# Kernel tuning notes

Hardware: AMD Instinct MI355X
Metric: run time of the kernel (lower is better)

Reference implementation:

```python
import jax, jax.numpy as jnp
import numpy as np

HEADS = 16
D_MODEL = 1024
GROUP = 4
SEQ = 2048
HEAD_DIM = D_MODEL // HEADS          # 64
KV_HEADS = HEADS // GROUP            # 4


def rope_tables(head_dim, seq_len, base=10000.0):
    # NOTE: faithful to source: exp = -2*arange(0,d,2)/d  (steps of 2 -> base^{-4j/d})
    exp = -2.0 * jnp.arange(0, head_dim, 2, dtype=jnp.float32) / head_dim
    thetas = jnp.power(base, exp)                       # [d/2]
    m = jnp.arange(seq_len, dtype=jnp.float32)          # [S]
    freq = jnp.outer(m, thetas)                         # [S, d/2]
    return jnp.cos(freq), jnp.sin(freq)


def apply_rope(x, cos, sin):
    # x: [B,S,H,D]; complex rotation on consecutive pairs
    B, S, H, D = x.shape
    xr = x.reshape(B, S, H, D // 2, 2)
    x0, x1 = xr[..., 0], xr[..., 1]
    c = cos[None, :S, None, :]
    s = sin[None, :S, None, :]
    out = jnp.stack([x0 * c - x1 * s, x0 * s + x1 * c], axis=-1)
    return out.reshape(B, S, H, D)


def setup_inputs() -> dict:
    key = jax.random.key(0)
    ks = jax.random.split(key, 8)
    B = 1
    q = jax.random.normal(ks[0], (B, SEQ, D_MODEL), dtype=jnp.float32)
    k = jax.random.normal(ks[1], (B, SEQ, D_MODEL), dtype=jnp.float32)
    v = jax.random.normal(ks[2], (B, SEQ, D_MODEL), dtype=jnp.float32)
    mask = jnp.tril(jnp.ones((SEQ, SEQ), dtype=jnp.int32))[None]  # causal [B,S,S]
    sc = 0.02
    Wq = jax.random.normal(ks[3], (D_MODEL, D_MODEL), dtype=jnp.float32) * sc
    Wk = jax.random.normal(ks[4], (D_MODEL, D_MODEL // GROUP), dtype=jnp.float32) * sc
    Wv = jax.random.normal(ks[5], (D_MODEL, D_MODEL // GROUP), dtype=jnp.float32) * sc
    Wo = jax.random.normal(ks[6], (D_MODEL, D_MODEL), dtype=jnp.float32) * sc
    bq = jnp.zeros((D_MODEL,), jnp.float32)
    bk = jnp.zeros((D_MODEL // GROUP,), jnp.float32)
    bv = jnp.zeros((D_MODEL // GROUP,), jnp.float32)
    bo = jnp.zeros((D_MODEL,), jnp.float32)
    return {"q": q, "k": k, "v": v, "mask": mask, "Wq": Wq, "bq": bq,
            "Wk": Wk, "bk": bk, "Wv": Wv, "bv": bv, "Wo": Wo, "bo": bo}


def reference(q, k, v, mask, Wq, bq, Wk, bk, Wv, bv, Wo, bo):
    B, S, _ = q.shape
    cos, sin = rope_tables(HEAD_DIM, S)
    qh = (q @ Wq + bq).reshape(B, S, HEADS, HEAD_DIM)
    kh = (k @ Wk + bk).reshape(B, S, KV_HEADS, HEAD_DIM)
    vh = (v @ Wv + bv).reshape(B, S, KV_HEADS, HEAD_DIM)
    qh = apply_rope(qh, cos, sin)
    kh = apply_rope(kh, cos, sin)
    qh = qh.transpose(0, 2, 1, 3)                       # [B,H,S,D]
    kh = kh.transpose(0, 2, 1, 3)                       # [B,Hkv,S,D]
    vh = vh.transpose(0, 2, 1, 3)
    # torch .repeat tiles: query head j attends kv head j % KV_HEADS
    kh = jnp.tile(kh, (1, GROUP, 1, 1))                 # [B,H,S,D]
    vh = jnp.tile(vh, (1, GROUP, 1, 1))
    scores = jnp.einsum('bhqd,bhkd->bhqk', qh, kh) / jnp.sqrt(
        jnp.asarray(HEAD_DIM, dtype=qh.dtype))
    scores = jnp.where(mask[:, None, :, :] == 0, -jnp.inf, scores)
    attn = jax.nn.softmax(scores, axis=-1)
    out = jnp.einsum('bhqk,bhkd->bhqd', attn, vh)
    out = out.transpose(0, 2, 1, 3).reshape(B, S, D_MODEL)
    return out @ Wo + bo
```

## Files before the change

kernel.cpp:

```cpp
#include <hip/hip_runtime.h>
#include <hip/hip_bf16.h>
#include <math.h>


#define SEQ 2048
#define DM 1024
#define HD 64

using u16 = unsigned short;
typedef __attribute__((ext_vector_type(8))) short bf16x8;
typedef __attribute__((ext_vector_type(4))) float f32x4;

#define QSCALE 0.18033688011112042f

__device__ __forceinline__ u16 f2b(float f) {
    union { float f; unsigned int i; } v; v.f = f;
    unsigned int u = v.i;
    return (u16)((u + 0x7fffu + ((u >> 16) & 1u)) >> 16);
}
__device__ __forceinline__ u16 f2b_fast(float f) {
    union { float f; unsigned int i; } v; v.f = f;
    return (u16)((v.i + 0x8000u) >> 16);
}

__global__ __launch_bounds__(256) void prep_kernel(
    const float* __restrict__ qin, const float* __restrict__ kin, const float* __restrict__ vin,
    const float* __restrict__ Wq, const float* __restrict__ Wk,
    const float* __restrict__ Wv, const float* __restrict__ Wo,
    u16* __restrict__ Xq, u16* __restrict__ Xk, u16* __restrict__ Xv,
    u16* __restrict__ Wt, u16* __restrict__ wot)
{
    const int b = blockIdx.x;
    const int t = threadIdx.x;

    if (b < 640) {
        __shared__ short T[64][72];
        const float* W; u16* dst; int N, t0, rowoff;
        if (b < 256)      { W = Wq; dst = Wt;  N = 1024; t0 = b;       rowoff = 0; }
        else if (b < 320) { W = Wk; dst = Wt;  N = 256;  t0 = b - 256; rowoff = 1024; }
        else if (b < 384) { W = Wv; dst = Wt;  N = 256;  t0 = b - 320; rowoff = 1280; }
        else              { W = Wo; dst = wot; N = 1024; t0 = b - 384; rowoff = 0; }
        const int ntn = N >> 6;
        const int k0 = (t0 / ntn) * 64, n0 = (t0 % ntn) * 64;
        const int r = t >> 4, c4 = (t & 15) * 4;
        #pragma unroll
        for (int rr = 0; rr < 4; ++rr) {
            const int k = r + rr * 16;
            float4 w4 = *reinterpret_cast<const float4*>(W + (size_t)(k0 + k) * N + n0 + c4);
            T[c4 + 0][k] = (short)f2b(w4.x);
            T[c4 + 1][k] = (short)f2b(w4.y);
            T[c4 + 2][k] = (short)f2b(w4.z);
            T[c4 + 3][k] = (short)f2b(w4.w);
        }
        __syncthreads();
        const int n = t >> 2, ck = (t & 3) * 16;
        u16* dp = dst + (size_t)(rowoff + n0 + n) * DM + k0 + ck;
        *reinterpret_cast<bf16x8*>(dp)     = *reinterpret_cast<const bf16x8*>(&T[n][ck]);
        *reinterpret_cast<bf16x8*>(dp + 8) = *reinterpret_cast<const bf16x8*>(&T[n][ck + 8]);
    } else {
        const int idx = b - 640;
        const int which = idx >> 8;
        const int ib = idx & 255;
        const float* src = (which == 0) ? qin : (which == 1) ? kin : vin;
        u16* dst = (which == 0) ? Xq : (which == 1) ? Xk : Xv;
        const size_t base = (size_t)ib * 8192 + (size_t)t * 32;
        #pragma unroll
        for (int c = 0; c < 4; ++c) {
            float4 x0 = *reinterpret_cast<const float4*>(src + base + c * 8);
            float4 x1 = *reinterpret_cast<const float4*>(src + base + c * 8 + 4);
            bf16x8 o;
            o[0] = (short)f2b(x0.x); o[1] = (short)f2b(x0.y);
            o[2] = (short)f2b(x0.z); o[3] = (short)f2b(x0.w);
            o[4] = (short)f2b(x1.x); o[5] = (short)f2b(x1.y);
            o[6] = (short)f2b(x1.z); o[7] = (short)f2b(x1.w);
            *reinterpret_cast<bf16x8*>(dst + base + c * 8) = o;
        }
    }
}

__global__ __launch_bounds__(256) void proj_mfma(
    const u16* __restrict__ Xq, const u16* __restrict__ Xk, const u16* __restrict__ Xv,
    const u16* __restrict__ Wt,
    const float* __restrict__ bq, const float* __restrict__ bk, const float* __restrict__ bv,
    u16* __restrict__ Qr, u16* __restrict__ Kr, u16* __restrict__ Vrt)
{
    const int n0 = blockIdx.x * 64, m0 = blockIdx.y * 64;
    const int zone = (n0 < 1024) ? 0 : (n0 < 1280) ? 1 : 2;
    const u16* __restrict__ Az = (zone == 0) ? Xq : (zone == 1) ? Xk : Xv;

    __shared__ short As[2][64][72];
    __shared__ short Bs[2][64][72];

    const int t = threadIdx.x;
    const int w = t >> 6, lane = t & 63, lm = lane & 15, quad = lane >> 4;
    const int sr = t >> 2, sc = (t & 3) * 16;

    f32x4 acc[4] = { {0,0,0,0}, {0,0,0,0}, {0,0,0,0}, {0,0,0,0} };

    const u16* ap_ = Az + (size_t)(m0 + sr) * DM + sc;
    const u16* bp_ = Wt + (size_t)(n0 + sr) * DM + sc;
    bf16x8 aR0 = *reinterpret_cast<const bf16x8*>(ap_);
    bf16x8 aR1 = *reinterpret_cast<const bf16x8*>(ap_ + 8);
    bf16x8 bR0 = *reinterpret_cast<const bf16x8*>(bp_);
    bf16x8 bR1 = *reinterpret_cast<const bf16x8*>(bp_ + 8);

    for (int k0 = 0; k0 < DM; k0 += 64) {
        const int buf = (k0 >> 6) & 1;
        *reinterpret_cast<bf16x8*>(&As[buf][sr][sc])     = aR0;
        *reinterpret_cast<bf16x8*>(&As[buf][sr][sc + 8]) = aR1;
        *reinterpret_cast<bf16x8*>(&Bs[buf][sr][sc])     = bR0;
        *reinterpret_cast<bf16x8*>(&Bs[buf][sr][sc + 8]) = bR1;
        if (k0 + 64 < DM) {
            aR0 = *reinterpret_cast<const bf16x8*>(ap_ + k0 + 64);
            aR1 = *reinterpret_cast<const bf16x8*>(ap_ + k0 + 72);
            bR0 = *reinterpret_cast<const bf16x8*>(bp_ + k0 + 64);
            bR1 = *reinterpret_cast<const bf16x8*>(bp_ + k0 + 72);
        }
        __syncthreads();
        bf16x8 af0 = *reinterpret_cast<const bf16x8*>(&As[buf][16 * w + lm][quad * 8]);
        bf16x8 af1 = *reinterpret_cast<const bf16x8*>(&As[buf][16 * w + lm][32 + quad * 8]);
        #pragma unroll
        for (int nb = 0; nb < 4; ++nb) {
            bf16x8 b0 = *reinterpret_cast<const bf16x8*>(&Bs[buf][16 * nb + lm][quad * 8]);
            bf16x8 b1 = *reinterpret_cast<const bf16x8*>(&Bs[buf][16 * nb + lm][32 + quad * 8]);
            acc[nb] = __builtin_amdgcn_mfma_f32_16x16x32_bf16(af0, b0, acc[nb], 0, 0, 0);
            acc[nb] = __builtin_amdgcn_mfma_f32_16x16x32_bf16(af1, b1, acc[nb], 0, 0, 0);
        }
        __syncthreads();
    }

    const float* __restrict__ bias = (zone == 0) ? bq : (zone == 1) ? bk : bv;
    const int nbase = (zone == 0) ? n0 : (zone == 1) ? (n0 - 1024) : (n0 - 1280);
    const int head = nbase >> 6;
    #pragma unroll
    for (int nb = 0; nb < 4; ++nb) {
        const int d = 16 * nb + lm;
        const float bvv = bias[nbase + d];
        float vals[4];
        #pragma unroll
        for (int r = 0; r < 4; ++r) vals[r] = acc[nb][r] + bvv;
        if (zone != 2) {
            const int pi = d >> 1;
            const float theta = exp2f(-0.8304820237f * (float)pi);
            const bool odd = (lm & 1);
            const float sca = (zone == 0) ? QSCALE : 1.0f;
            u16* op = (zone == 0 ? Qr : Kr) + (size_t)head * SEQ * HD;
            #pragma unroll
            for (int r = 0; r < 4; ++r) {
                const int m = m0 + 16 * w + quad * 4 + r;
                float sn, cs;
                sincosf((float)m * theta, &sn, &cs);
                float x  = vals[r];
                float xp = __shfl_xor(x, 1);
                float o  = (odd ? (xp * sn + x * cs) : (x * cs - xp * sn)) * sca;
                op[(size_t)m * HD + d] = f2b(o);
            }
        } else {
            u16* vp = Vrt + ((size_t)head * HD + d) * SEQ;
            #pragma unroll
            for (int r = 0; r < 4; ++r) {
                const int m = m0 + 16 * w + quad * 4 + r;
                const int within = m & 63;
                const int pos = (m & ~63) + 4 * (within & 15) + (within >> 4);
                vp[pos] = f2b(vals[r]);
            }
        }
    }
}

__global__ __launch_bounds__(512) void attn_mfma(
    const u16* __restrict__ Qr, const u16* __restrict__ Kr, const u16* __restrict__ Vrt,
    u16* __restrict__ AO)
{
    const int h  = blockIdx.x;
    const int qy = blockIdx.y;
    const int kvh = h & 3;

    __shared__ u16 Ks[2][64][72];
    __shared__ u16 Vt[2][64][72];
    __shared__ u16 Ps[8][16][76];

    const int t = threadIdx.x;
    const int w = t >> 6, lane = t & 63, lm = lane & 15, quad = lane >> 4;
    const int team = w >> 2, wt = w & 3;
    const int qt  = team ? (31 - qy) : qy;
    const int qtb = 31 - qy;

    {
        const int row = lane >> 2, c = (lane & 3) * 16;
        const u16* qp = Qr + ((size_t)h * SEQ + qt * 64 + wt * 16 + row) * HD + c;
        *reinterpret_cast<bf16x8*>(&Ps[w][row][c])     = *reinterpret_cast<const bf16x8*>(qp);
        *reinterpret_cast<bf16x8*>(&Ps[w][row][c + 8]) = *reinterpret_cast<const bf16x8*>(qp + 8);
    }
    const bf16x8 aq0 = *reinterpret_cast<const bf16x8*>(&Ps[w][lm][quad * 8]);
    const bf16x8 aq1 = *reinterpret_cast<const bf16x8*>(&Ps[w][lm][32 + quad * 8]);

    f32x4 O[4] = { {0,0,0,0}, {0,0,0,0}, {0,0,0,0}, {0,0,0,0} };
    float lp[4] = { 0.f, 0.f, 0.f, 0.f };

    const int srow = t >> 3, sc2 = (t & 7) * 8;
    const u16* kb_ = Kr  + ((size_t)kvh * SEQ + srow) * HD + sc2;
    const u16* vb_ = Vrt + ((size_t)kvh * HD + srow) * SEQ + sc2;
    bf16x8 kR = *reinterpret_cast<const bf16x8*>(kb_);
    bf16x8 vR = *reinterpret_cast<const bf16x8*>(vb_);

    for (int kt = 0; kt <= qtb; ++kt) {
        const int buf = kt & 1;
        *reinterpret_cast<bf16x8*>(&Ks[buf][srow][sc2]) = kR;
        *reinterpret_cast<bf16x8*>(&Vt[buf][srow][sc2]) = vR;
        if (kt < qtb) {
            kR = *reinterpret_cast<const bf16x8*>(kb_ + (size_t)(kt + 1) * 64 * HD);
            vR = *reinterpret_cast<const bf16x8*>(vb_ + (size_t)(kt + 1) * 64);
        }
        __syncthreads();

        if (kt <= qt) {
            f32x4 s[4];
            #pragma unroll
            for (int nb = 0; nb < 4; ++nb) {
                bf16x8 b0 = *reinterpret_cast<const bf16x8*>(&Ks[buf][16 * nb + lm][quad * 8]);
                bf16x8 b1 = *reinterpret_cast<const bf16x8*>(&Ks[buf][16 * nb + lm][32 + quad * 8]);
                f32x4 zz = { 0.f, 0.f, 0.f, 0.f };
                zz = __builtin_amdgcn_mfma_f32_16x16x32_bf16(aq0, b0, zz, 0, 0, 0);
                s[nb] = __builtin_amdgcn_mfma_f32_16x16x32_bf16(aq1, b1, zz, 0, 0, 0);
            }

            if (kt == qt) {
                #pragma unroll
                for (int nb = 0; nb < 4; ++nb)
                    #pragma unroll
                    for (int r = 0; r < 4; ++r)
                        if (16 * nb + lm > 16 * wt + quad * 4 + r) s[nb][r] = -INFINITY;
            }

            #pragma unroll
            for (int r = 0; r < 4; ++r) {
                u16 pk[4];
                #pragma unroll
                for (int nb = 0; nb < 4; ++nb) {
                    float e = __builtin_amdgcn_exp2f(fminf(s[nb][r], 126.f));
                    lp[r] += e;
                    pk[nb] = f2b_fast(e);
                }
                *reinterpret_cast<uint2*>(&Ps[w][quad * 4 + r][4 * lm]) =
                    *reinterpret_cast<uint2*>(pk);
            }

            const bf16x8 ap0 = *reinterpret_cast<const bf16x8*>(&Ps[w][lm][quad * 8]);
            const bf16x8 ap1 = *reinterpret_cast<const bf16x8*>(&Ps[w][lm][32 + quad * 8]);
            #pragma unroll
            for (int db = 0; db < 4; ++db) {
                bf16x8 v0 = *reinterpret_cast<const bf16x8*>(&Vt[buf][16 * db + lm][quad * 8]);
                bf16x8 v1 = *reinterpret_cast<const bf16x8*>(&Vt[buf][16 * db + lm][32 + quad * 8]);
                O[db] = __builtin_amdgcn_mfma_f32_16x16x32_bf16(ap0, v0, O[db], 0, 0, 0);
                O[db] = __builtin_amdgcn_mfma_f32_16x16x32_bf16(ap1, v1, O[db], 0, 0, 0);
            }
        }
    }

    #pragma unroll
    for (int r = 0; r < 4; ++r) {
        #pragma unroll
        for (int off = 1; off < 16; off <<= 1)
            lp[r] += __shfl_xor(lp[r], off);
        const float inv = 1.0f / lp[r];
        const size_t row = (size_t)(qt * 64 + 16 * wt + quad * 4 + r) * DM + (size_t)h * HD;
        #pragma unroll
        for (int db = 0; db < 4; ++db)
            AO[row + 16 * db + lm] = f2b(O[db][r] * inv);
    }
}

__global__ __launch_bounds__(256) void oproj_mfma(
    const u16* __restrict__ AO, const u16* __restrict__ wot,
    const float* __restrict__ bo, float* __restrict__ out)
{
    __shared__ short As[2][64][72];
    __shared__ short Bs[2][64][72];
    const int t = threadIdx.x;
    const int w = t >> 6, lane = t & 63, lm = lane & 15, quad = lane >> 4;
    const int m0 = blockIdx.y * 64, n0 = blockIdx.x * 64;
    const int sr = t >> 2, sc = (t & 3) * 16;

    f32x4 acc[4] = { {0,0,0,0}, {0,0,0,0}, {0,0,0,0}, {0,0,0,0} };

    const u16* ap_ = AO  + (size_t)(m0 + sr) * DM + sc;
    const u16* bp_ = wot + (size_t)(n0 + sr) * DM + sc;
    bf16x8 aR0 = *reinterpret_cast<const bf16x8*>(ap_);
    bf16x8 aR1 = *reinterpret_cast<const bf16x8*>(ap_ + 8);
    bf16x8 bR0 = *reinterpret_cast<const bf16x8*>(bp_);
    bf16x8 bR1 = *reinterpret_cast<const bf16x8*>(bp_ + 8);

    for (int k0 = 0; k0 < DM; k0 += 64) {
        const int buf = (k0 >> 6) & 1;
        *reinterpret_cast<bf16x8*>(&As[buf][sr][sc])     = aR0;
        *reinterpret_cast<bf16x8*>(&As[buf][sr][sc + 8]) = aR1;
        *reinterpret_cast<bf16x8*>(&Bs[buf][sr][sc])     = bR0;
        *reinterpret_cast<bf16x8*>(&Bs[buf][sr][sc + 8]) = bR1;
        if (k0 + 64 < DM) {
            aR0 = *reinterpret_cast<const bf16x8*>(ap_ + k0 + 64);
            aR1 = *reinterpret_cast<const bf16x8*>(ap_ + k0 + 72);
            bR0 = *reinterpret_cast<const bf16x8*>(bp_ + k0 + 64);
            bR1 = *reinterpret_cast<const bf16x8*>(bp_ + k0 + 72);
        }
        __syncthreads();
        bf16x8 af0 = *reinterpret_cast<const bf16x8*>(&As[buf][16 * w + lm][quad * 8]);
        bf16x8 af1 = *reinterpret_cast<const bf16x8*>(&As[buf][16 * w + lm][32 + quad * 8]);
        #pragma unroll
        for (int nb = 0; nb < 4; ++nb) {
            bf16x8 b0 = *reinterpret_cast<const bf16x8*>(&Bs[buf][16 * nb + lm][quad * 8]);
            bf16x8 b1 = *reinterpret_cast<const bf16x8*>(&Bs[buf][16 * nb + lm][32 + quad * 8]);
            acc[nb] = __builtin_amdgcn_mfma_f32_16x16x32_bf16(af0, b0, acc[nb], 0, 0, 0);
            acc[nb] = __builtin_amdgcn_mfma_f32_16x16x32_bf16(af1, b1, acc[nb], 0, 0, 0);
        }
        __syncthreads();
    }

    #pragma unroll
    for (int nb = 0; nb < 4; ++nb) {
        const int dl = 16 * nb + lm;
        const float bv = bo[n0 + dl];
        #pragma unroll
        for (int r = 0; r < 4; ++r) {
            const int m = m0 + 16 * w + quad * 4 + r;
            out[(size_t)m * DM + n0 + dl] = acc[nb][r] + bv;
        }
    }
}

extern "C" void kernel_launch(void* const* d_in, const int* in_sizes, int n_in,
                              void* d_out, int out_size, void* d_ws, size_t ws_size,
                              hipStream_t stream)
{
    const float* q  = (const float*)d_in[0];
    const float* k  = (const float*)d_in[1];
    const float* v  = (const float*)d_in[2];
    const float* Wq = (const float*)d_in[4];
    const float* bq = (const float*)d_in[5];
    const float* Wk = (const float*)d_in[6];
    const float* bk = (const float*)d_in[7];
    const float* Wv = (const float*)d_in[8];
    const float* bv = (const float*)d_in[9];
    const float* Wo = (const float*)d_in[10];
    const float* bo = (const float*)d_in[11];
    float* out = (float*)d_out;

    u16* Xq  = (u16*)d_ws;
    u16* Xk  = Xq  + (size_t)SEQ * DM;
    u16* Xv  = Xk  + (size_t)SEQ * DM;
    u16* Wt  = Xv  + (size_t)SEQ * DM;
    u16* wot = Wt  + (size_t)1536 * 1024;
    u16* Qr  = wot + (size_t)1024 * 1024;
    u16* Kr  = Qr  + (size_t)16 * SEQ * HD;
    u16* Vrt = Kr  + (size_t)4 * SEQ * HD;
    u16* AO  = Vrt + (size_t)4 * SEQ * HD;

    hipLaunchKernelGGL(prep_kernel, dim3(1408), dim3(256), 0, stream,
                       q, k, v, Wq, Wk, Wv, Wo, Xq, Xk, Xv, Wt, wot);
    hipLaunchKernelGGL(proj_mfma, dim3(24, 32), dim3(256), 0, stream,
                       Xq, Xk, Xv, Wt, bq, bk, bv, Qr, Kr, Vrt);
    hipLaunchKernelGGL(attn_mfma, dim3(16, 16), dim3(512), 0, stream,
                       Qr, Kr, Vrt, AO);
    hipLaunchKernelGGL(oproj_mfma, dim3(16, 32), dim3(256), 0, stream,
                       AO, wot, bo, out);
}
```

Before: 166.3 us.

## Split attention KV tiles across two warp teams per query tile; drop redundant GEMM syncs

The attention kernel now assigns one query tile per block, 512 blocks in total. The two 4-warp teams process alternating KV tiles of that query tile, and their partial O and row sums are merged through shared memory at the end. This replaces the old scheme, where the teams worked on paired query tiles sharing a KV stream. The aim is more parallelism and an even causal split, at the cost of dropping the register prefetch of K/V, adding two barriers per iteration and a reduction step. Separately, the trailing __syncthreads in the double-buffered projection and output-projection GEMM loops is removed, which stays safe because each buffer is rewritten only after a later barrier.

```diff
diff --git a/kernel.cpp b/kernel.cpp
--- a/kernel.cpp
+++ b/kernel.cpp
@@ -126,7 +126,6 @@
             acc[nb] = __builtin_amdgcn_mfma_f32_16x16x32_bf16(af0, b0, acc[nb], 0, 0, 0);
             acc[nb] = __builtin_amdgcn_mfma_f32_16x16x32_bf16(af1, b1, acc[nb], 0, 0, 0);
         }
-        __syncthreads();
     }
 
     const float* __restrict__ bias = (zone == 0) ? bq : (zone == 1) ? bk : bv;
@@ -173,8 +172,11 @@
     u16* __restrict__ AO)
 {
     const int h  = blockIdx.x;
-    const int qy = blockIdx.y;
+    const int y  = blockIdx.y;
+    const int qt = (y < 16) ? (2 * y) : (63 - 2 * y);
     const int kvh = h & 3;
+    const int ntile = qt + 1;
+    const int nIter = (ntile + 1) >> 1;
 
     __shared__ u16 Ks[2][64][72];
     __shared__ u16 Vt[2][64][72];
@@ -183,17 +185,10 @@
     const int t = threadIdx.x;
     const int w = t >> 6, lane = t & 63, lm = lane & 15, quad = lane >> 4;
     const int team = w >> 2, wt = w & 3;
-    const int qt  = team ? (31 - qy) : qy;
-    const int qtb = 31 - qy;
-
-    {
-        const int row = lane >> 2, c = (lane & 3) * 16;
-        const u16* qp = Qr + ((size_t)h * SEQ + qt * 64 + wt * 16 + row) * HD + c;
-        *reinterpret_cast<bf16x8*>(&Ps[w][row][c])     = *reinterpret_cast<const bf16x8*>(qp);
-        *reinterpret_cast<bf16x8*>(&Ps[w][row][c + 8]) = *reinterpret_cast<const bf16x8*>(qp + 8);
-    }
-    const bf16x8 aq0 = *reinterpret_cast<const bf16x8*>(&Ps[w][lm][quad * 8]);
-    const bf16x8 aq1 = *reinterpret_cast<const bf16x8*>(&Ps[w][lm][32 + quad * 8]);
+
+    const u16* qp = Qr + ((size_t)h * SEQ + qt * 64 + 16 * wt + lm) * HD + quad * 8;
+    const bf16x8 aq0 = *reinterpret_cast<const bf16x8*>(qp);
+    const bf16x8 aq1 = *reinterpret_cast<const bf16x8*>(qp + 32);
 
     f32x4 O[4] = { {0,0,0,0}, {0,0,0,0}, {0,0,0,0}, {0,0,0,0} };
     float lp[4] = { 0.f, 0.f, 0.f, 0.f };
@@ -201,25 +196,28 @@
     const int srow = t >> 3, sc2 = (t & 7) * 8;
     const u16* kb_ = Kr  + ((size_t)kvh * SEQ + srow) * HD + sc2;
     const u16* vb_ = Vrt + ((size_t)kvh * HD + srow) * SEQ + sc2;
-    bf16x8 kR = *reinterpret_cast<const bf16x8*>(kb_);
-    bf16x8 vR = *reinterpret_cast<const bf16x8*>(vb_);
-
-    for (int kt = 0; kt <= qtb; ++kt) {
-        const int buf = kt & 1;
-        *reinterpret_cast<bf16x8*>(&Ks[buf][srow][sc2]) = kR;
-        *reinterpret_cast<bf16x8*>(&Vt[buf][srow][sc2]) = vR;
-        if (kt < qtb) {
-            kR = *reinterpret_cast<const bf16x8*>(kb_ + (size_t)(kt + 1) * 64 * HD);
-            vR = *reinterpret_cast<const bf16x8*>(vb_ + (size_t)(kt + 1) * 64);
-        }
-        __syncthreads();
-
-        if (kt <= qt) {
+
+    u16* ps = &Ps[w][0][0];
+
+    for (int i = 0; i < nIter; ++i) {
+        const int kt0 = 2 * i;
+        *reinterpret_cast<bf16x8*>(&Ks[0][srow][sc2]) =
+            *reinterpret_cast<const bf16x8*>(kb_ + (size_t)(kt0 * 64) * HD);
+        *reinterpret_cast<bf16x8*>(&Ks[1][srow][sc2]) =
+            *reinterpret_cast<const bf16x8*>(kb_ + (size_t)(kt0 * 64 + 64) * HD);
+        *reinterpret_cast<bf16x8*>(&Vt[0][srow][sc2]) =
+            *reinterpret_cast<const bf16x8*>(vb_ + (size_t)(kt0 * 64));
+        *reinterpret_cast<bf16x8*>(&Vt[1][srow][sc2]) =
+            *reinterpret_cast<const bf16x8*>(vb_ + (size_t)(kt0 * 64 + 64));
+        __syncthreads();
+
+        const int kt = kt0 + team;
+        if (kt < ntile) {
             f32x4 s[4];
             #pragma unroll
             for (int nb = 0; nb < 4; ++nb) {
-                bf16x8 b0 = *reinterpret_cast<const bf16x8*>(&Ks[buf][16 * nb + lm][quad * 8]);
-                bf16x8 b1 = *reinterpret_cast<const bf16x8*>(&Ks[buf][16 * nb + lm][32 + quad * 8]);
+                bf16x8 b0 = *reinterpret_cast<const bf16x8*>(&Ks[team][16 * nb + lm][quad * 8]);
+                bf16x8 b1 = *reinterpret_cast<const bf16x8*>(&Ks[team][16 * nb + lm][32 + quad * 8]);
                 f32x4 zz = { 0.f, 0.f, 0.f, 0.f };
                 zz = __builtin_amdgcn_mfma_f32_16x16x32_bf16(aq0, b0, zz, 0, 0, 0);
                 s[nb] = __builtin_amdgcn_mfma_f32_16x16x32_bf16(aq1, b1, zz, 0, 0, 0);
@@ -242,32 +240,53 @@
                     lp[r] += e;
                     pk[nb] = f2b_fast(e);
                 }
-                *reinterpret_cast<uint2*>(&Ps[w][quad * 4 + r][4 * lm]) =
+                *reinterpret_cast<uint2*>(&ps[(quad * 4 + r) * 76 + 4 * lm]) =
                     *reinterpret_cast<uint2*>(pk);
             }
 
-            const bf16x8 ap0 = *reinterpret_cast<const bf16x8*>(&Ps[w][lm][quad * 8]);
-            const bf16x8 ap1 = *reinterpret_cast<const bf16x8*>(&Ps[w][lm][32 + quad * 8]);
+            const bf16x8 ap0 = *reinterpret_cast<const bf16x8*>(&ps[lm * 76 + quad * 8]);
+            const bf16x8 ap1 = *reinterpret_cast<const bf16x8*>(&ps[lm * 76 + 32 + quad * 8]);
             #pragma unroll
             for (int db = 0; db < 4; ++db) {
-                bf16x8 v0 = *reinterpret_cast<const bf16x8*>(&Vt[buf][16 * db + lm][quad * 8]);
-                bf16x8 v1 = *reinterpret_cast<const bf16x8*>(&Vt[buf][16 * db + lm][32 + quad * 8]);
+                bf16x8 v0 = *reinterpret_cast<const bf16x8*>(&Vt[team][16 * db + lm][quad * 8]);
+                bf16x8 v1 = *reinterpret_cast<const bf16x8*>(&Vt[team][16 * db + lm][32 + quad * 8]);
                 O[db] = __builtin_amdgcn_mfma_f32_16x16x32_bf16(ap0, v0, O[db], 0, 0, 0);
                 O[db] = __builtin_amdgcn_mfma_f32_16x16x32_bf16(ap1, v1, O[db], 0, 0, 0);
             }
         }
-    }
-
-    #pragma unroll
-    for (int r = 0; r < 4; ++r) {
-        #pragma unroll
-        for (int off = 1; off < 16; off <<= 1)
-            lp[r] += __shfl_xor(lp[r], off);
-        const float inv = 1.0f / lp[r];
-        const size_t row = (size_t)(qt * 64 + 16 * wt + quad * 4 + r) * DM + (size_t)h * HD;
-        #pragma unroll
-        for (int db = 0; db < 4; ++db)
-            AO[row + 16 * db + lm] = f2b(O[db][r] * inv);
+        __syncthreads();
+    }
+
+    float* Obuf = reinterpret_cast<float*>(&Ks[0][0][0]);
+    float* Lbuf = reinterpret_cast<float*>(&Vt[0][0][0]);
+    if (team == 1) {
+        #pragma unroll
+        for (int r = 0; r < 4; ++r) {
+            const int row = wt * 16 + quad * 4 + r;
+            #pragma unroll
+            for (int db = 0; db < 4; ++db)
+                Obuf[row * 68 + 16 * db + lm] = O[db][r];
+            Lbuf[row * 16 + lm] = lp[r];
+        }
+    }
+    __syncthreads();
+    if (team == 0) {
+        #pragma unroll
+        for (int r = 0; r < 4; ++r) {
+            const int row = wt * 16 + quad * 4 + r;
+            #pragma unroll
+            for (int db = 0; db < 4; ++db)
+                O[db][r] += Obuf[row * 68 + 16 * db + lm];
+            lp[r] += Lbuf[row * 16 + lm];
+            #pragma unroll
+            for (int off = 1; off < 16; off <<= 1)
+                lp[r] += __shfl_xor(lp[r], off);
+            const float inv = 1.0f / lp[r];
+            const size_t orow = (size_t)(qt * 64 + row) * DM + (size_t)h * HD;
+            #pragma unroll
+            for (int db = 0; db < 4; ++db)
+                AO[orow + 16 * db + lm] = f2b(O[db][r] * inv);
+        }
     }
 }
 
@@ -313,7 +332,6 @@
             acc[nb] = __builtin_amdgcn_mfma_f32_16x16x32_bf16(af0, b0, acc[nb], 0, 0, 0);
             acc[nb] = __builtin_amdgcn_mfma_f32_16x16x32_bf16(af1, b1, acc[nb], 0, 0, 0);
         }
-        __syncthreads();
     }
 
     #pragma unroll
@@ -359,7 +377,7 @@
                        q, k, v, Wq, Wk, Wv, Wo, Xq, Xk, Xv, Wt, wot);
     hipLaunchKernelGGL(proj_mfma, dim3(24, 32), dim3(256), 0, stream,
                        Xq, Xk, Xv, Wt, bq, bk, bv, Qr, Kr, Vrt);
-    hipLaunchKernelGGL(attn_mfma, dim3(16, 16), dim3(512), 0, stream,
+    hipLaunchKernelGGL(attn_mfma, dim3(16, 32), dim3(512), 0, stream,
                        Qr, Kr, Vrt, AO);
     hipLaunchKernelGGL(oproj_mfma, dim3(16, 32), dim3(256), 0, stream,
                        AO, wot, bo, out);
```

After: 170.0 us. 1.02x slower.

## Fuse all four stages into one persistent cooperative kernel with grid syncs

Applied to the files above, without the earlier changes.

Replaces the four separate launches (prep, projection, attention, output projection) with a single cooperative kernel of 512 blocks that loops over work units per stage and separates stages with grid.sync. Attention is remapped from 16x16 blocks of 512 threads with paired query tiles to 512 blocks of 256 threads, one query tile each with balanced ordering. The GEMM loops also drop the trailing __syncthreads. The aim is to remove launch gaps and inter-kernel drain. The cost is grid-barrier overhead, a fixed 2-blocks-per-CU occupancy limit, and possibly worse load balance in the causal attention stage.

```diff
diff --git a/kernel.cpp b/kernel.cpp
--- a/kernel.cpp
+++ b/kernel.cpp
@@ -1,6 +1,9 @@
 #include <hip/hip_runtime.h>
+#include <hip/hip_cooperative_groups.h>
 #include <hip/hip_bf16.h>
 #include <math.h>
+
+namespace cg = cooperative_groups;
 
 
 #define SEQ 2048
@@ -23,198 +26,203 @@
     return (u16)((v.i + 0x8000u) >> 16);
 }
 
-__global__ __launch_bounds__(256) void prep_kernel(
+__global__ __launch_bounds__(256, 2) void fused_kernel(
     const float* __restrict__ qin, const float* __restrict__ kin, const float* __restrict__ vin,
     const float* __restrict__ Wq, const float* __restrict__ Wk,
     const float* __restrict__ Wv, const float* __restrict__ Wo,
+    const float* __restrict__ bq, const float* __restrict__ bk,
+    const float* __restrict__ bv, const float* __restrict__ bo,
     u16* __restrict__ Xq, u16* __restrict__ Xk, u16* __restrict__ Xv,
-    u16* __restrict__ Wt, u16* __restrict__ wot)
+    u16* __restrict__ Wt, u16* __restrict__ wot,
+    u16* __restrict__ Qr, u16* __restrict__ Kr, u16* __restrict__ Vrt,
+    u16* __restrict__ AO, float* __restrict__ out)
 {
-    const int b = blockIdx.x;
-    const int t = threadIdx.x;
-
-    if (b < 640) {
-        __shared__ short T[64][72];
-        const float* W; u16* dst; int N, t0, rowoff;
-        if (b < 256)      { W = Wq; dst = Wt;  N = 1024; t0 = b;       rowoff = 0; }
-        else if (b < 320) { W = Wk; dst = Wt;  N = 256;  t0 = b - 256; rowoff = 1024; }
-        else if (b < 384) { W = Wv; dst = Wt;  N = 256;  t0 = b - 320; rowoff = 1280; }
-        else              { W = Wo; dst = wot; N = 1024; t0 = b - 384; rowoff = 0; }
-        const int ntn = N >> 6;
-        const int k0 = (t0 / ntn) * 64, n0 = (t0 % ntn) * 64;
-        const int r = t >> 4, c4 = (t & 15) * 4;
-        #pragma unroll
-        for (int rr = 0; rr < 4; ++rr) {
-            const int k = r + rr * 16;
-            float4 w4 = *reinterpret_cast<const float4*>(W + (size_t)(k0 + k) * N + n0 + c4);
-            T[c4 + 0][k] = (short)f2b(w4.x);
-            T[c4 + 1][k] = (short)f2b(w4.y);
-            T[c4 + 2][k] = (short)f2b(w4.z);
-            T[c4 + 3][k] = (short)f2b(w4.w);
-        }
-        __syncthreads();
-        const int n = t >> 2, ck = (t & 3) * 16;
-        u16* dp = dst + (size_t)(rowoff + n0 + n) * DM + k0 + ck;
-        *reinterpret_cast<bf16x8*>(dp)     = *reinterpret_cast<const bf16x8*>(&T[n][ck]);
-        *reinterpret_cast<bf16x8*>(dp + 8) = *reinterpret_cast<const bf16x8*>(&T[n][ck + 8]);
-    } else {
-        const int idx = b - 640;
-        const int which = idx >> 8;
-        const int ib = idx & 255;
-        const float* src = (which == 0) ? qin : (which == 1) ? kin : vin;
-        u16* dst = (which == 0) ? Xq : (which == 1) ? Xk : Xv;
-        const size_t base = (size_t)ib * 8192 + (size_t)t * 32;
-        #pragma unroll
-        for (int c = 0; c < 4; ++c) {
-            float4 x0 = *reinterpret_cast<const float4*>(src + base + c * 8);
-            float4 x1 = *reinterpret_cast<const float4*>(src + base + c * 8 + 4);
-            bf16x8 o;
-            o[0] = (short)f2b(x0.x); o[1] = (short)f2b(x0.y);
-            o[2] = (short)f2b(x0.z); o[3] = (short)f2b(x0.w);
-            o[4] = (short)f2b(x1.x); o[5] = (short)f2b(x1.y);
-            o[6] = (short)f2b(x1.z); o[7] = (short)f2b(x1.w);
-            *reinterpret_cast<bf16x8*>(dst + base + c * 8) = o;
-        }
-    }
-}
-
-__global__ __launch_bounds__(256) void proj_mfma(
-    const u16* __restrict__ Xq, const u16* __restrict__ Xk, const u16* __restrict__ Xv,
-    const u16* __restrict__ Wt,
-    const float* __restrict__ bq, const float* __restrict__ bk, const float* __restrict__ bv,
-    u16* __restrict__ Qr, u16* __restrict__ Kr, u16* __restrict__ Vrt)
-{
-    const int n0 = blockIdx.x * 64, m0 = blockIdx.y * 64;
-    const int zone = (n0 < 1024) ? 0 : (n0 < 1280) ? 1 : 2;
-    const u16* __restrict__ Az = (zone == 0) ? Xq : (zone == 1) ? Xk : Xv;
-
-    __shared__ short As[2][64][72];
-    __shared__ short Bs[2][64][72];
-
+    cg::grid_group grid = cg::this_grid();
+
+    __shared__ __align__(16) u16 smem[23296];
+
+    const int bid = blockIdx.x;
     const int t = threadIdx.x;
     const int w = t >> 6, lane = t & 63, lm = lane & 15, quad = lane >> 4;
-    const int sr = t >> 2, sc = (t & 3) * 16;
-
-    f32x4 acc[4] = { {0,0,0,0}, {0,0,0,0}, {0,0,0,0}, {0,0,0,0} };
-
-    const u16* ap_ = Az + (size_t)(m0 + sr) * DM + sc;
-    const u16* bp_ = Wt + (size_t)(n0 + sr) * DM + sc;
-    bf16x8 aR0 = *reinterpret_cast<const bf16x8*>(ap_);
-    bf16x8 aR1 = *reinterpret_cast<const bf16x8*>(ap_ + 8);
-    bf16x8 bR0 = *reinterpret_cast<const bf16x8*>(bp_);
-    bf16x8 bR1 = *reinterpret_cast<const bf16x8*>(bp_ + 8);
-
-    for (int k0 = 0; k0 < DM; k0 += 64) {
-        const int buf = (k0 >> 6) & 1;
-        *reinterpret_cast<bf16x8*>(&As[buf][sr][sc])     = aR0;
-        *reinterpret_cast<bf16x8*>(&As[buf][sr][sc + 8]) = aR1;
-        *reinterpret_cast<bf16x8*>(&Bs[buf][sr][sc])     = bR0;
-        *reinterpret_cast<bf16x8*>(&Bs[buf][sr][sc + 8]) = bR1;
-        if (k0 + 64 < DM) {
-            aR0 = *reinterpret_cast<const bf16x8*>(ap_ + k0 + 64);
-            aR1 = *reinterpret_cast<const bf16x8*>(ap_ + k0 + 72);
-            bR0 = *reinterpret_cast<const bf16x8*>(bp_ + k0 + 64);
-            bR1 = *reinterpret_cast<const bf16x8*>(bp_ + k0 + 72);
-        }
-        __syncthreads();
-        bf16x8 af0 = *reinterpret_cast<const bf16x8*>(&As[buf][16 * w + lm][quad * 8]);
-        bf16x8 af1 = *reinterpret_cast<const bf16x8*>(&As[buf][16 * w + lm][32 + quad * 8]);
-        #pragma unroll
-        for (int nb = 0; nb < 4; ++nb) {
-            bf16x8 b0 = *reinterpret_cast<const bf16x8*>(&Bs[buf][16 * nb + lm][quad * 8]);
-            bf16x8 b1 = *reinterpret_cast<const bf16x8*>(&Bs[buf][16 * nb + lm][32 + quad * 8]);
-            acc[nb] = __builtin_amdgcn_mfma_f32_16x16x32_bf16(af0, b0, acc[nb], 0, 0, 0);
-            acc[nb] = __builtin_amdgcn_mfma_f32_16x16x32_bf16(af1, b1, acc[nb], 0, 0, 0);
-        }
-        __syncthreads();
+
+    {
+        short (*T)[72] = (short(*)[72])smem;
+        for (int u = bid; u < 1408; u += 512) {
+            __syncthreads();
+            if (u < 640) {
+                const float* W; u16* dst; int N, t0, rowoff;
+                if (u < 256)      { W = Wq; dst = Wt;  N = 1024; t0 = u;       rowoff = 0; }
+                else if (u < 320) { W = Wk; dst = Wt;  N = 256;  t0 = u - 256; rowoff = 1024; }
+                else if (u < 384) { W = Wv; dst = Wt;  N = 256;  t0 = u - 320; rowoff = 1280; }
+                else              { W = Wo; dst = wot; N = 1024; t0 = u - 384; rowoff = 0; }
+                const int ntn = N >> 6;
+                const int k0 = (t0 / ntn) * 64, n0 = (t0 % ntn) * 64;
+                const int r = t >> 4, c4 = (t & 15) * 4;
+                #pragma unroll
+                for (int rr = 0; rr < 4; ++rr) {
+                    const int k = r + rr * 16;
+                    float4 w4 = *reinterpret_cast<const float4*>(W + (size_t)(k0 + k) * N + n0 + c4);
+                    T[c4 + 0][k] = (short)f2b(w4.x);
+                    T[c4 + 1][k] = (short)f2b(w4.y);
+                    T[c4 + 2][k] = (short)f2b(w4.z);
+                    T[c4 + 3][k] = (short)f2b(w4.w);
+                }
+                __syncthreads();
+                const int n = t >> 2, ck = (t & 3) * 16;
+                u16* dp = dst + (size_t)(rowoff + n0 + n) * DM + k0 + ck;
+                *reinterpret_cast<bf16x8*>(dp)     = *reinterpret_cast<const bf16x8*>(&T[n][ck]);
+                *reinterpret_cast<bf16x8*>(dp + 8) = *reinterpret_cast<const bf16x8*>(&T[n][ck + 8]);
+            } else {
+                const int idx = u - 640;
+                const int which = idx >> 8;
+                const int ib = idx & 255;
+                const float* src = (which == 0) ? qin : (which == 1) ? kin : vin;
+                u16* dst = (which == 0) ? Xq : (which == 1) ? Xk : Xv;
+                const size_t base = (size_t)ib * 8192 + (size_t)t * 32;
+                #pragma unroll
+                for (int c = 0; c < 4; ++c) {
+                    float4 x0 = *reinterpret_cast<const float4*>(src + base + c * 8);
+                    float4 x1 = *reinterpret_cast<const float4*>(src + base + c * 8 + 4);
+                    bf16x8 o;
+                    o[0] = (short)f2b(x0.x); o[1] = (short)f2b(x0.y);
+                    o[2] = (short)f2b(x0.z); o[3] = (short)f2b(x0.w);
+                    o[4] = (short)f2b(x1.x); o[5] = (short)f2b(x1.y);
+                    o[6] = (short)f2b(x1.z); o[7] = (short)f2b(x1.w);
+                    *reinterpret_cast<bf16x8*>(dst + base + c * 8) = o;
+                }
+            }
+        }
     }
-
-    const float* __restrict__ bias = (zone == 0) ? bq : (zone == 1) ? bk : bv;
-    const int nbase = (zone == 0) ? n0 : (zone == 1) ? (n0 - 1024) : (n0 - 1280);
-    const int head = nbase >> 6;
-    #pragma unroll
-    for (int nb = 0; nb < 4; ++nb) {
-        const int d = 16 * nb + lm;
-        const float bvv = bias[nbase + d];
-        float vals[4];
-        #pragma unroll
-        for (int r = 0; r < 4; ++r) vals[r] = acc[nb][r] + bvv;
-        if (zone != 2) {
-            const int pi = d >> 1;
-            const float theta = exp2f(-0.8304820237f * (float)pi);
-            const bool odd = (lm & 1);
-            const float sca = (zone == 0) ? QSCALE : 1.0f;
-            u16* op = (zone == 0 ? Qr : Kr) + (size_t)head * SEQ * HD;
-            #pragma unroll
-            for (int r = 0; r < 4; ++r) {
-                const int m = m0 + 16 * w + quad * 4 + r;
-                float sn, cs;
-                sincosf((float)m * theta, &sn, &cs);
-                float x  = vals[r];
-                float xp = __shfl_xor(x, 1);
-                float o  = (odd ? (xp * sn + x * cs) : (x * cs - xp * sn)) * sca;
-                op[(size_t)m * HD + d] = f2b(o);
-            }
-        } else {
-            u16* vp = Vrt + ((size_t)head * HD + d) * SEQ;
-            #pragma unroll
-            for (int r = 0; r < 4; ++r) {
-                const int m = m0 + 16 * w + quad * 4 + r;
-                const int within = m & 63;
-                const int pos = (m & ~63) + 4 * (within & 15) + (within >> 4);
-                vp[pos] = f2b(vals[r]);
+    grid.sync();
+
+    {
+        u16 (*As)[64][72] = (u16(*)[64][72])smem;
+        u16 (*Bs)[64][72] = (u16(*)[64][72])(smem + 9216);
+        const int sr = t >> 2, sc = (t & 3) * 16;
+
+        for (int u = bid; u < 768; u += 512) {
+            __syncthreads();
+            const int n0 = (u % 24) * 64, m0 = (u / 24) * 64;
+            const int zone = (n0 < 1024) ? 0 : (n0 < 1280) ? 1 : 2;
+            const u16* __restrict__ Az = (zone == 0) ? Xq : (zone == 1) ? Xk : Xv;
+
+            f32x4 acc[4] = { {0,0,0,0}, {0,0,0,0}, {0,0,0,0}, {0,0,0,0} };
+
+            const u16* ap_ = Az + (size_t)(m0 + sr) * DM + sc;
+            const u16* bp_ = Wt + (size_t)(n0 + sr) * DM + sc;
+            bf16x8 aR0 = *reinterpret_cast<const bf16x8*>(ap_);
+            bf16x8 aR1 = *reinterpret_cast<const bf16x8*>(ap_ + 8);
+            bf16x8 bR0 = *reinterpret_cast<const bf16x8*>(bp_);
+            bf16x8 bR1 = *reinterpret_cast<const bf16x8*>(bp_ + 8);
+
+            for (int k0 = 0; k0 < DM; k0 += 64) {
+                const int buf = (k0 >> 6) & 1;
+                *reinterpret_cast<bf16x8*>(&As[buf][sr][sc])     = aR0;
+                *reinterpret_cast<bf16x8*>(&As[buf][sr][sc + 8]) = aR1;
+                *reinterpret_cast<bf16x8*>(&Bs[buf][sr][sc])     = bR0;
+                *reinterpret_cast<bf16x8*>(&Bs[buf][sr][sc + 8]) = bR1;
+                if (k0 + 64 < DM) {
+                    aR0 = *reinterpret_cast<const bf16x8*>(ap_ + k0 + 64);
+                    aR1 = *reinterpret_cast<const bf16x8*>(ap_ + k0 + 72);
+                    bR0 = *reinterpret_cast<const bf16x8*>(bp_ + k0 + 64);
+                    bR1 = *reinterpret_cast<const bf16x8*>(bp_ + k0 + 72);
+                }
+                __syncthreads();
+                bf16x8 af0 = *reinterpret_cast<const bf16x8*>(&As[buf][16 * w + lm][quad * 8]);
+                bf16x8 af1 = *reinterpret_cast<const bf16x8*>(&As[buf][16 * w + lm][32 + quad * 8]);
+                #pragma unroll
+                for (int nb = 0; nb < 4; ++nb) {
+                    bf16x8 b0 = *reinterpret_cast<const bf16x8*>(&Bs[buf][16 * nb + lm][quad * 8]);
+                    bf16x8 b1 = *reinterpret_cast<const bf16x8*>(&Bs[buf][16 * nb + lm][32 + quad * 8]);
+                    acc[nb] = __builtin_amdgcn_mfma_f32_16x16x32_bf16(af0, b0, acc[nb], 0, 0, 0);
+                    acc[nb] = __builtin_amdgcn_mfma_f32_16x16x32_bf16(af1, b1, acc[nb], 0, 0, 0);
+                }
+            }
+
+            const float* __restrict__ bias = (zone == 0) ? bq : (zone == 1) ? bk : bv;
+            const int nbase = (zone == 0) ? n0 : (zone == 1) ? (n0 - 1024) : (n0 - 1280);
+            const int head = nbase >> 6;
+            #pragma unroll
+            for (int nb = 0; nb < 4; ++nb) {
+                const int d = 16 * nb + lm;
+                const float bvv = bias[nbase + d];
+                float vals[4];
+                #pragma unroll
+                for (int r = 0; r < 4; ++r) vals[r] = acc[nb][r] + bvv;
+                if (zone != 2) {
+                    const int pi = d >> 1;
+                    const float theta = exp2f(-0.8304820237f * (float)pi);
+                    const bool odd = (lm & 1);
+                    const float sca = (zone == 0) ? QSCALE : 1.0f;
+                    u16* op = (zone == 0 ? Qr : Kr) + (size_t)head * SEQ * HD;
+                    #pragma unroll
+                    for (int r = 0; r < 4; ++r) {
+                        const int m = m0 + 16 * w + quad * 4 + r;
+                        float sn, cs;
+                        sincosf((float)m * theta, &sn, &cs);
+                        float x  = vals[r];
+                        float xp = __shfl_xor(x, 1);
+                        float o  = (odd ? (xp * sn + x * cs) : (x * cs - xp * sn)) * sca;
+                        op[(size_t)m * HD + d] = f2b(o);
+                    }
+                } else {
+                    u16* vp = Vrt + ((size_t)head * HD + d) * SEQ;
+                    #pragma unroll
+                    for (int r = 0; r < 4; ++r) {
+                        const int m = m0 + 16 * w + quad * 4 + r;
+                        const int within = m & 63;
+                        const int pos = (m & ~63) + 4 * (within & 15) + (within >> 4);
+                        vp[pos] = f2b(vals[r]);
+                    }
+                }
             }
         }
     }
-}
-
-__global__ __launch_bounds__(512) void attn_mfma(
-    const u16* __restrict__ Qr, const u16* __restrict__ Kr, const u16* __restrict__ Vrt,
-    u16* __restrict__ AO)
-{
-    const int h  = blockIdx.x;
-    const int qy = blockIdx.y;
-    const int kvh = h & 3;
-
-    __shared__ u16 Ks[2][64][72];
-    __shared__ u16 Vt[2][64][72];
-    __shared__ u16 Ps[8][16][76];
-
-    const int t = threadIdx.x;
-    const int w = t >> 6, lane = t & 63, lm = lane & 15, quad = lane >> 4;
-    const int team = w >> 2, wt = w & 3;
-    const int qt  = team ? (31 - qy) : qy;
-    const int qtb = 31 - qy;
+    grid.sync();
 
     {
-        const int row = lane >> 2, c = (lane & 3) * 16;
-        const u16* qp = Qr + ((size_t)h * SEQ + qt * 64 + wt * 16 + row) * HD + c;
-        *reinterpret_cast<bf16x8*>(&Ps[w][row][c])     = *reinterpret_cast<const bf16x8*>(qp);
-        *reinterpret_cast<bf16x8*>(&Ps[w][row][c + 8]) = *reinterpret_cast<const bf16x8*>(qp + 8);
-    }
-    const bf16x8 aq0 = *reinterpret_cast<const bf16x8*>(&Ps[w][lm][quad * 8]);
-    const bf16x8 aq1 = *reinterpret_cast<const bf16x8*>(&Ps[w][lm][32 + quad * 8]);
-
-    f32x4 O[4] = { {0,0,0,0}, {0,0,0,0}, {0,0,0,0}, {0,0,0,0} };
-    float lp[4] = { 0.f, 0.f, 0.f, 0.f };
-
-    const int srow = t >> 3, sc2 = (t & 7) * 8;
-    const u16* kb_ = Kr  + ((size_t)kvh * SEQ + srow) * HD + sc2;
-    const u16* vb_ = Vrt + ((size_t)kvh * HD + srow) * SEQ + sc2;
-    bf16x8 kR = *reinterpret_cast<const bf16x8*>(kb_);
-    bf16x8 vR = *reinterpret_cast<const bf16x8*>(vb_);
-
-    for (int kt = 0; kt <= qtb; ++kt) {
-        const int buf = kt & 1;
-        *reinterpret_cast<bf16x8*>(&Ks[buf][srow][sc2]) = kR;
-        *reinterpret_cast<bf16x8*>(&Vt[buf][srow][sc2]) = vR;
-        if (kt < qtb) {
-            kR = *reinterpret_cast<const bf16x8*>(kb_ + (size_t)(kt + 1) * 64 * HD);
-            vR = *reinterpret_cast<const bf16x8*>(vb_ + (size_t)(kt + 1) * 64);
-        }
-        __syncthreads();
-
-        if (kt <= qt) {
+        u16 (*Ks)[64][72] = (u16(*)[64][72])smem;
+        u16 (*Vt)[64][72] = (u16(*)[64][72])(smem + 9216);
+        u16 (*Ps)[16][76] = (u16(*)[16][76])(smem + 18432);
+
+        const int h = bid & 15;
+        const int idx = bid >> 4;
+        const int qt = (idx < 16) ? idx : 47 - idx;
+        const int kvh = h & 3;
+
+        const u16* qp = Qr + ((size_t)h * SEQ + qt * 64 + 16 * w + lm) * HD + quad * 8;
+        const bf16x8 aq0 = *reinterpret_cast<const bf16x8*>(qp);
+        const bf16x8 aq1 = *reinterpret_cast<const bf16x8*>(qp + 32);
+
+        f32x4 O[4] = { {0,0,0,0}, {0,0,0,0}, {0,0,0,0}, {0,0,0,0} };
+        float lp[4] = { 0.f, 0.f, 0.f, 0.f };
+
+        const int sr = t >> 2, sc = (t & 3) * 16;
+        const u16* kb_ = Kr  + ((size_t)kvh * SEQ + sr) * HD + sc;
+        const u16* vb_ = Vrt + ((size_t)kvh * HD + sr) * SEQ + sc;
+        bf16x8 kR0 = *reinterpret_cast<const bf16x8*>(kb_);
+        bf16x8 kR1 = *reinterpret_cast<const bf16x8*>(kb_ + 8);
+        bf16x8 vR0 = *reinterpret_cast<const bf16x8*>(vb_);
+        bf16x8 vR1 = *reinterpret_cast<const bf16x8*>(vb_ + 8);
+
+        u16* ps = &Ps[w][0][0];
+
+        for (int kt = 0; kt <= qt; ++kt) {
+            const int buf = kt & 1;
+            *reinterpret_cast<bf16x8*>(&Ks[buf][sr][sc])     = kR0;
+            *reinterpret_cast<bf16x8*>(&Ks[buf][sr][sc + 8]) = kR1;
+            *reinterpret_cast<bf16x8*>(&Vt[buf][sr][sc])     = vR0;
+            *reinterpret_cast<bf16x8*>(&Vt[buf][sr][sc + 8]) = vR1;
+            if (kt < qt) {
+                const u16* kp = kb_ + (size_t)(kt + 1) * 64 * HD;
+                const u16* vp = vb_ + (size_t)(kt + 1) * 64;
+                kR0 = *reinterpret_cast<const bf16x8*>(kp);
+                kR1 = *reinterpret_cast<const bf16x8*>(kp + 8);
+                vR0 = *reinterpret_cast<const bf16x8*>(vp);
+                vR1 = *reinterpret_cast<const bf16x8*>(vp + 8);
+            }
+            __syncthreads();
+
             f32x4 s[4];
             #pragma unroll
             for (int nb = 0; nb < 4; ++nb) {
@@ -230,7 +238,7 @@
                 for (int nb = 0; nb < 4; ++nb)
                     #pragma unroll
                     for (int r = 0; r < 4; ++r)
-                        if (16 * nb + lm > 16 * wt + quad * 4 + r) s[nb][r] = -INFINITY;
+                        if (16 * nb + lm > 16 * w + quad * 4 + r) s[nb][r] = -INFINITY;
             }
 
             #pragma unroll
@@ -242,12 +250,12 @@
                     lp[r] += e;
                     pk[nb] = f2b_fast(e);
                 }
-                *reinterpret_cast<uint2*>(&Ps[w][quad * 4 + r][4 * lm]) =
+                *reinterpret_cast<uint2*>(&ps[(quad * 4 + r) * 76 + 4 * lm]) =
                     *reinterpret_cast<uint2*>(pk);
             }
 
-            const bf16x8 ap0 = *reinterpret_cast<const bf16x8*>(&Ps[w][lm][quad * 8]);
-            const bf16x8 ap1 = *reinterpret_cast<const bf16x8*>(&Ps[w][lm][32 + quad * 8]);
+            const bf16x8 ap0 = *reinterpret_cast<const bf16x8*>(&ps[lm * 76 + quad * 8]);
+            const bf16x8 ap1 = *reinterpret_cast<const bf16x8*>(&ps[lm * 76 + 32 + quad * 8]);
             #pragma unroll
             for (int db = 0; db < 4; ++db) {
                 bf16x8 v0 = *reinterpret_cast<const bf16x8*>(&Vt[buf][16 * db + lm][quad * 8]);
@@ -256,74 +264,69 @@
                 O[db] = __builtin_amdgcn_mfma_f32_16x16x32_bf16(ap1, v1, O[db], 0, 0, 0);
             }
         }
+
+        #pragma unroll
+        for (int r = 0; r < 4; ++r) {
+            #pragma unroll
+            for (int off = 1; off < 16; off <<= 1)
+                lp[r] += __shfl_xor(lp[r], off);
+            const float inv = 1.0f / lp[r];
+            const size_t orow = (size_t)(qt * 64 + 16 * w + quad * 4 + r) * DM + (size_t)h * HD;
+            #pragma unroll
+            for (int db = 0; db < 4; ++db)
+                AO[orow + 16 * db + lm] = f2b(O[db][r] * inv);
+        }
     }
-
-    #pragma unroll
-    for (int r = 0; r < 4; ++r) {
-        #pragma unroll
-        for (int off = 1; off < 16; off <<= 1)
-            lp[r] += __shfl_xor(lp[r], off);
-        const float inv = 1.0f / lp[r];
-        const size_t row = (size_t)(qt * 64 + 16 * wt + quad * 4 + r) * DM + (size_t)h * HD;
-        #pragma unroll
-        for (int db = 0; db < 4; ++db)
-            AO[row + 16 * db + lm] = f2b(O[db][r] * inv);
-    }
-}
-
-__global__ __launch_bounds__(256) void oproj_mfma(
-    const u16* __restrict__ AO, const u16* __restrict__ wot,
-    const float* __restrict__ bo, float* __restrict__ out)
-{
-    __shared__ short As[2][64][72];
-    __shared__ short Bs[2][64][72];
-    const int t = threadIdx.x;
-    const int w = t >> 6, lane = t & 63, lm = lane & 15, quad = lane >> 4;
-    const int m0 = blockIdx.y * 64, n0 = blockIdx.x * 64;
-    const int sr = t >> 2, sc = (t & 3) * 16;
-
-    f32x4 acc[4] = { {0,0,0,0}, {0,0,0,0}, {0,0,0,0}, {0,0,0,0} };
-
-    const u16* ap_ = AO  + (size_t)(m0 + sr) * DM + sc;
-    const u16* bp_ = wot + (size_t)(n0 + sr) * DM + sc;
-    bf16x8 aR0 = *reinterpret_cast<const bf16x8*>(ap_);
-    bf16x8 aR1 = *reinterpret_cast<const bf16x8*>(ap_ + 8);
-    bf16x8 bR0 = *reinterpret_cast<const bf16x8*>(bp_);
-    bf16x8 bR1 = *reinterpret_cast<const bf16x8*>(bp_ + 8);
-
-    for (int k0 = 0; k0 < DM; k0 += 64) {
-        const int buf = (k0 >> 6) & 1;
-        *reinterpret_cast<bf16x8*>(&As[buf][sr][sc])     = aR0;
-        *reinterpret_cast<bf16x8*>(&As[buf][sr][sc + 8]) = aR1;
-        *reinterpret_cast<bf16x8*>(&Bs[buf][sr][sc])     = bR0;
-        *reinterpret_cast<bf16x8*>(&Bs[buf][sr][sc + 8]) = bR1;
-        if (k0 + 64 < DM) {
-            aR0 = *reinterpret_cast<const bf16x8*>(ap_ + k0 + 64);
-            aR1 = *reinterpret_cast<const bf16x8*>(ap_ + k0 + 72);
-            bR0 = *reinterpret_cast<const bf16x8*>(bp_ + k0 + 64);
-            bR1 = *reinterpret_cast<const bf16x8*>(bp_ + k0 + 72);
-        }
-        __syncthreads();
-        bf16x8 af0 = *reinterpret_cast<const bf16x8*>(&As[buf][16 * w + lm][quad * 8]);
-        bf16x8 af1 = *reinterpret_cast<const bf16x8*>(&As[buf][16 * w + lm][32 + quad * 8]);
+    grid.sync();
+
+    {
+        u16 (*As)[64][72] = (u16(*)[64][72])smem;
+        u16 (*Bs)[64][72] = (u16(*)[64][72])(smem + 9216);
+        const int sr = t >> 2, sc = (t & 3) * 16;
+        const int n0 = (bid & 15) * 64, m0 = (bid >> 4) * 64;
+
+        f32x4 acc[4] = { {0,0,0,0}, {0,0,0,0}, {0,0,0,0}, {0,0,0,0} };
+
+        const u16* ap_ = AO  + (size_t)(m0 + sr) * DM + sc;
+        const u16* bp_ = wot + (size_t)(n0 + sr) * DM + sc;
+        bf16x8 aR0 = *reinterpret_cast<const bf16x8*>(ap_);
+        bf16x8 aR1 = *reinterpret_cast<const bf16x8*>(ap_ + 8);
+        bf16x8 bR0 = *reinterpret_cast<const bf16x8*>(bp_);
+        bf16x8 bR1 = *reinterpret_cast<const bf16x8*>(bp_ + 8);
+
+        for (int k0 = 0; k0 < DM; k0 += 64) {
+            const int buf = (k0 >> 6) & 1;
+            *reinterpret_cast<bf16x8*>(&As[buf][sr][sc])     = aR0;
+            *reinterpret_cast<bf16x8*>(&As[buf][sr][sc + 8]) = aR1;
+            *reinterpret_cast<bf16x8*>(&Bs[buf][sr][sc])     = bR0;
+            *reinterpret_cast<bf16x8*>(&Bs[buf][sr][sc + 8]) = bR1;
+            if (k0 + 64 < DM) {
+                aR0 = *reinterpret_cast<const bf16x8*>(ap_ + k0 + 64);
+                aR1 = *reinterpret_cast<const bf16x8*>(ap_ + k0 + 72);
+                bR0 = *reinterpret_cast<const bf16x8*>(bp_ + k0 + 64);
+                bR1 = *reinterpret_cast<const bf16x8*>(bp_ + k0 + 72);
+            }
+            __syncthreads();
+            bf16x8 af0 = *reinterpret_cast<const bf16x8*>(&As[buf][16 * w + lm][quad * 8]);
+            bf16x8 af1 = *reinterpret_cast<const bf16x8*>(&As[buf][16 * w + lm][32 + quad * 8]);
+            #pragma unroll
+            for (int nb = 0; nb < 4; ++nb) {
+                bf16x8 b0 = *reinterpret_cast<const bf16x8*>(&Bs[buf][16 * nb + lm][quad * 8]);
+                bf16x8 b1 = *reinterpret_cast<const bf16x8*>(&Bs[buf][16 * nb + lm][32 + quad * 8]);
+                acc[nb] = __builtin_amdgcn_mfma_f32_16x16x32_bf16(af0, b0, acc[nb], 0, 0, 0);
+                acc[nb] = __builtin_amdgcn_mfma_f32_16x16x32_bf16(af1, b1, acc[nb], 0, 0, 0);
+            }
+        }
+
         #pragma unroll
         for (int nb = 0; nb < 4; ++nb) {
-            bf16x8 b0 = *reinterpret_cast<const bf16x8*>(&Bs[buf][16 * nb + lm][quad * 8]);
-            bf16x8 b1 = *reinterpret_cast<const bf16x8*>(&Bs[buf][16 * nb + lm][32 + quad * 8]);
-            acc[nb] = __builtin_amdgcn_mfma_f32_16x16x32_bf16(af0, b0, acc[nb], 0, 0, 0);
-            acc[nb] = __builtin_amdgcn_mfma_f32_16x16x32_bf16(af1, b1, acc[nb], 0, 0, 0);
-        }
-        __syncthreads();
-    }
-
-    #pragma unroll
-    for (int nb = 0; nb < 4; ++nb) {
-        const int dl = 16 * nb + lm;
-        const float bv = bo[n0 + dl];
-        #pragma unroll
-        for (int r = 0; r < 4; ++r) {
-            const int m = m0 + 16 * w + quad * 4 + r;
-            out[(size_t)m * DM + n0 + dl] = acc[nb][r] + bv;
+            const int dl = 16 * nb + lm;
+            const float bvv = bo[n0 + dl];
+            #pragma unroll
+            for (int r = 0; r < 4; ++r) {
+                const int m = m0 + 16 * w + quad * 4 + r;
+                out[(size_t)m * DM + n0 + dl] = acc[nb][r] + bvv;
+            }
         }
     }
 }
@@ -355,12 +358,13 @@
     u16* Vrt = Kr  + (size_t)4 * SEQ * HD;
     u16* AO  = Vrt + (size_t)4 * SEQ * HD;
 
-    hipLaunchKernelGGL(prep_kernel, dim3(1408), dim3(256), 0, stream,
-                       q, k, v, Wq, Wk, Wv, Wo, Xq, Xk, Xv, Wt, wot);
-    hipLaunchKernelGGL(proj_mfma, dim3(24, 32), dim3(256), 0, stream,
-                       Xq, Xk, Xv, Wt, bq, bk, bv, Qr, Kr, Vrt);
-    hipLaunchKernelGGL(attn_mfma, dim3(16, 16), dim3(512), 0, stream,
-                       Qr, Kr, Vrt, AO);
-    hipLaunchKernelGGL(oproj_mfma, dim3(16, 32), dim3(256), 0, stream,
-                       AO, wot, bo, out);
+    void* args[] = {
+        (void*)&q, (void*)&k, (void*)&v,
+        (void*)&Wq, (void*)&Wk, (void*)&Wv, (void*)&Wo,
+        (void*)&bq, (void*)&bk, (void*)&bv, (void*)&bo,
+        (void*)&Xq, (void*)&Xk, (void*)&Xv, (void*)&Wt, (void*)&wot,
+        (void*)&Qr, (void*)&Kr, (void*)&Vrt, (void*)&AO, (void*)&out
+    };
+    hipLaunchCooperativeKernel((const void*)fused_kernel, dim3(512), dim3(256),
+                               args, 0, stream);
 }
```

Result: slower. 394.4 us (+137.2%).
